# Performance work log

Measured on AMD Instinct MI355X. Metric: run time of the kernel, lower is better.

Reference implementation:

```python
import jax, jax.numpy as jnp
import numpy as np

B, N, D, H, DK, DV, R = 4, 256, 256, 8, 32, 32, 64
EPS = 1e-6


def setup_inputs() -> dict:
    key = jax.random.key(0)
    ks = jax.random.split(key, 16)
    s = D ** -0.5
    return {
        "q": jax.random.normal(ks[0], (B, N, D), jnp.float32),
        "k": jax.random.normal(ks[1], (B, N, D), jnp.float32),
        "v": jax.random.normal(ks[2], (B, N, D), jnp.float32),
        "mask": jax.random.randint(ks[3], (B, N, N), 0, 2).astype(jnp.int32),
        "link": jax.random.uniform(ks[4], (B, N, N, R), jnp.float32),
        "Wq": jax.random.normal(ks[5], (D, H * DK), jnp.float32) * s,
        "Wk": jax.random.normal(ks[6], (D, H * DK), jnp.float32) * s,
        "Wr": jax.random.normal(ks[7], (D, H * DK), jnp.float32) * s,
        "Wv": jax.random.normal(ks[8], (D, H * DV), jnp.float32) * s,
        "Wvv": jax.random.normal(ks[9], (D, H * DV), jnp.float32) * s,
        "relationE": jax.random.normal(ks[10], (R, D), jnp.float32) * s,
        "Wo": jax.random.normal(ks[11], (H * DV, D), jnp.float32) * s,
        "gamma": jnp.ones((D,), jnp.float32),
        "beta": jnp.zeros((D,), jnp.float32),
    }


def reference(q, k, v, mask, link, Wq, Wk, Wr, Wv, Wvv, relationE, Wo, gamma, beta):
    # rela_num != 0 branch of Ruleformer MultiHeadAttention (dropout = identity, eval mode).
    residual = q
    b, n, d = q.shape
    # per-head projections of X (== q == residual in this branch): [b,h,n,dk]
    Xq = (q @ Wq).reshape(b, n, H, DK).transpose(0, 2, 1, 3)
    Xk = (q @ Wk).reshape(b, n, H, DK).transpose(0, 2, 1, 3)
    Xv = (q @ Wv).reshape(b, n, H, DV).transpose(0, 2, 1, 3)

    # calcE: relation-biased scores. Rk[b,i,j,h,d] = (link @ relationE @ Wr)
    Rk = jnp.einsum('bijr,re->bije', link, relationE @ Wr).reshape(b, n, n, H, DK)
    # attn[b,h,i,j] = Xq[b,h,i] . (Xk[b,h,j] + Rk[b,i,j,h])
    attn = jnp.einsum('bhid,bhjd->bhij', Xq, Xk)
    attn = attn + jnp.einsum('bijhd,bhid->bhij', Rk, Xq)
    attn = attn / (DK ** 0.5)
    attn = jnp.where(mask[:, None, :, :] == 0, -1e9, attn)
    alpha = jax.nn.softmax(attn, axis=-1)  # [b,h,n,n]

    # calcZ: Z[b,h,i] = sum_j alpha[b,h,i,j] * (Xv[b,h,j] + Rv[b,i,j,h])
    Rv = jnp.einsum('bijr,re->bije', link, relationE @ Wvv).reshape(b, n, n, H, DV)
    Z = jnp.einsum('bhij,bhjd->bhid', alpha, Xv)
    Z = Z + jnp.einsum('bhij,bijhd->bhid', alpha, Rv)

    out = Z.transpose(0, 2, 1, 3).reshape(b, n, H * DV) @ Wo
    out = out + residual
    mu = out.mean(-1, keepdims=True)
    var = ((out - mu) ** 2).mean(-1, keepdims=True)
    out = (out - mu) * jax.lax.rsqrt(var + EPS) * gamma + beta
    return out, alpha
```

## Files before the change

### kernel.cpp

```cpp
#include <hip/hip_runtime.h>
#include <math.h>

constexpr int B_ = 4, N_ = 256, D_ = 256, H_ = 8, DK_ = 32, DV_ = 32, R_ = 64;
constexpr float SCALE_ = 0.17677669529663687f;
constexpr float EPS_ = 1e-6f;

__global__ __launch_bounds__(256) void projekev_kernel(
        const float* __restrict__ q, const float* __restrict__ Wq,
        const float* __restrict__ Wk, const float* __restrict__ Wv,
        const float* __restrict__ relE, const float* __restrict__ Wr,
        const float* __restrict__ Wvv, float* __restrict__ Xq,
        float* __restrict__ Xk, float* __restrict__ Xv,
        float* __restrict__ Ek, float* __restrict__ Ev) {
    int blk = blockIdx.x;
    int t = threadIdx.x;
    __shared__ __align__(16) float ash[32 * 65];
    __shared__ __align__(16) float bsh[32 * 64];
    const float *src, *W;
    int rowbase, cbase, ct;
    float* dstE = nullptr;
    if (blk < 192) {
        ct = blk >> 4;
        int rt = blk & 15;
        src = q; rowbase = rt * 64;
        if (ct < 4)      { W = Wq; cbase = ct * 64; }
        else if (ct < 8) { W = Wk; cbase = (ct - 4) * 64; }
        else             { W = Wv; cbase = (ct - 8) * 64; }
    } else {
        int e = blk - 192;
        src = relE; rowbase = 0; ct = -1;
        W = (e < 4) ? Wr : Wvv;
        dstE = (e < 4) ? Ek : Ev;
        cbase = (e & 3) * 64;
    }
    int ti = t >> 4, tj = t & 15;
    float acc[4][4] = {{0.f}};
    for (int kc = 0; kc < 8; ++kc) {
        __syncthreads();
#pragma unroll
        for (int kk = 0; kk < 2; ++kk) {
            int m = t + kk * 256;
            int i = m >> 3, kq = m & 7;
            float4 v = *(const float4*)(src + (size_t)(rowbase + i) * 256 + kc * 32 + kq * 4);
            ash[(kq * 4 + 0) * 65 + i] = v.x;
            ash[(kq * 4 + 1) * 65 + i] = v.y;
            ash[(kq * 4 + 2) * 65 + i] = v.z;
            ash[(kq * 4 + 3) * 65 + i] = v.w;
        }
#pragma unroll
        for (int kk = 0; kk < 2; ++kk) {
            int m = t + kk * 256;
            int k = m >> 4, j4 = m & 15;
            float4 v = *(const float4*)(W + (size_t)(kc * 32 + k) * 256 + cbase + j4 * 4);
            *(float4*)(bsh + k * 64 + j4 * 4) = v;
        }
        __syncthreads();
#pragma unroll 8
        for (int k = 0; k < 32; ++k) {
            float4 av = *(const float4*)(ash + k * 65 + ti * 4);
            float4 bv = *(const float4*)(bsh + k * 64 + tj * 4);
            acc[0][0] += av.x * bv.x; acc[0][1] += av.x * bv.y;
            acc[0][2] += av.x * bv.z; acc[0][3] += av.x * bv.w;
            acc[1][0] += av.y * bv.x; acc[1][1] += av.y * bv.y;
            acc[1][2] += av.y * bv.z; acc[1][3] += av.y * bv.w;
            acc[2][0] += av.z * bv.x; acc[2][1] += av.z * bv.y;
            acc[2][2] += av.z * bv.z; acc[2][3] += av.z * bv.w;
            acc[3][0] += av.w * bv.x; acc[3][1] += av.w * bv.y;
            acc[3][2] += av.w * bv.z; acc[3][3] += av.w * bv.w;
        }
    }
    if (dstE) {
#pragma unroll
        for (int a = 0; a < 4; ++a) {
            int row = ti * 4 + a;
            *(float4*)(dstE + (size_t)row * 256 + cbase + tj * 4) =
                make_float4(acc[a][0], acc[a][1], acc[a][2], acc[a][3]);
        }
    } else {
        float* dst = (ct < 4) ? Xq : (ct < 8) ? Xk : Xv;
        int gcol = (ct & 3) * 64 + tj * 4;
        int h = gcol >> 5, dk = gcol & 31;
#pragma unroll
        for (int a = 0; a < 4; ++a) {
            int row = rowbase + ti * 4 + a;
            int bb = row >> 8, n = row & 255;
            *(float4*)(dst + ((size_t)(bb * 8 + h) * 256 + n) * 32 + dk) =
                make_float4(acc[a][0], acc[a][1], acc[a][2], acc[a][3]);
        }
    }
}

__global__ __launch_bounds__(256, 4) void biassmzout_kernel(
        const float* __restrict__ link, const float* __restrict__ Ek,
        const float* __restrict__ Ev, const float* __restrict__ Xq,
        const float* __restrict__ Xk, const float* __restrict__ Xv,
        const int* __restrict__ mask, const float* __restrict__ Wo,
        const float* __restrict__ q, const float* __restrict__ gamma,
        const float* __restrict__ beta, float* __restrict__ alpha,
        float* __restrict__ out) {
    int bi = ((blockIdx.x & 7) << 7) | (blockIdx.x >> 3);
    int b = bi >> 8, i = bi & 255;
    int t = threadIdx.x;
    int lane = t & 63, g = t >> 6;

    __shared__ __align__(16) float xqsh[256];
    __shared__ __align__(16) float Tsh[8 * 68];
    __shared__ __align__(16) float ashm[8 * 260];
    __shared__ __align__(16) float part[2048];
    __shared__ float redsh[64];

    float resid = q[(size_t)bi * 256 + t];
    int mv = mask[((size_t)(b * 256 + i)) * 256 + t];
    xqsh[t] = Xq[((size_t)(b * 8 + (t >> 5)) * 256 + i) * 32 + (t & 31)];
    __syncthreads();

#pragma unroll
    for (int hr = t; hr < 512; hr += 256) {
        int h = hr >> 6, r = hr & 63;
        const float4* e4 = (const float4*)(Ek + r * 256 + h * 32);
        const float4* x4 = (const float4*)(xqsh + h * 32);
        float acc = 0.f;
#pragma unroll
        for (int k = 0; k < 8; ++k) {
            float4 e = e4[k], x = x4[k];
            acc += e.x * x.x + e.y * x.y + e.z * x.z + e.w * x.w;
        }
        Tsh[h * 68 + r] = acc;
    }

    float s[8];
#pragma unroll 2
    for (int h = 0; h < 8; ++h) {
        const float4* k4 = (const float4*)(Xk + (((size_t)(b * 8 + h)) * 256 + t) * 32);
        const float4* x4 = (const float4*)(xqsh + h * 32);
        float acc = 0.f;
#pragma unroll
        for (int k = 0; k < 8; ++k) {
            float4 kv = k4[k], xv = x4[k];
            acc += kv.x * xv.x + kv.y * xv.y + kv.z * xv.z + kv.w * xv.w;
        }
        s[h] = acc;
    }
    __syncthreads();

    {
        const float4* l4 = (const float4*)(link + ((size_t)(bi * 256 + t)) * 64);
        const float4* T4 = (const float4*)Tsh;
#pragma unroll 8
        for (int k = 0; k < 16; ++k) {
            float4 lv = l4[k];
#pragma unroll
            for (int h = 0; h < 8; ++h) {
                float4 tv = T4[h * 17 + k];
                s[h] += lv.x * tv.x + lv.y * tv.y + lv.z * tv.z + lv.w * tv.w;
            }
        }
    }
#pragma unroll
    for (int h = 0; h < 8; ++h) {
        s[h] *= SCALE_;
        if (mv == 0) s[h] = -1e9f;
    }

#pragma unroll
    for (int h = 0; h < 8; ++h) {
        float v = s[h];
        for (int off = 32; off > 0; off >>= 1) v = fmaxf(v, __shfl_xor(v, off));
        if (lane == 0) redsh[h * 4 + g] = v;
    }
    __syncthreads();
    float mx[8];
#pragma unroll
    for (int h = 0; h < 8; ++h)
        mx[h] = fmaxf(fmaxf(redsh[h * 4 + 0], redsh[h * 4 + 1]),
                      fmaxf(redsh[h * 4 + 2], redsh[h * 4 + 3]));
#pragma unroll
    for (int h = 0; h < 8; ++h) {
        float e = __expf(s[h] - mx[h]);
        s[h] = e;
        float v = e;
        for (int off = 32; off > 0; off >>= 1) v += __shfl_xor(v, off);
        if (lane == 0) redsh[32 + h * 4 + g] = v;
    }
    __syncthreads();
#pragma unroll
    for (int h = 0; h < 8; ++h) {
        float esum = redsh[32 + h * 4 + 0] + redsh[32 + h * 4 + 1] +
                     redsh[32 + h * 4 + 2] + redsh[32 + h * 4 + 3];
        float a = s[h] * (1.f / esum);
        ashm[h * 260 + t] = a;
        alpha[((size_t)(b * 8 + h) * 256 + i) * 256 + t] = a;
    }
    __syncthreads();

    {
        float pacc[8] = {0.f, 0.f, 0.f, 0.f, 0.f, 0.f, 0.f, 0.f};
        const float* lp2 = link + ((size_t)(bi * 256 + g * 64)) * 64 + lane;
#pragma unroll 4
        for (int j4 = 0; j4 < 16; ++j4) {
            float l0 = lp2[(j4 * 4 + 0) * 64];
            float l1 = lp2[(j4 * 4 + 1) * 64];
            float l2 = lp2[(j4 * 4 + 2) * 64];
            float l3 = lp2[(j4 * 4 + 3) * 64];
#pragma unroll
            for (int h = 0; h < 8; ++h) {
                float4 a = *(const float4*)(ashm + h * 260 + g * 64 + j4 * 4);
                pacc[h] += a.x * l0 + a.y * l1 + a.z * l2 + a.w * l3;
            }
        }
#pragma unroll
        for (int h = 0; h < 8; ++h) part[g * 512 + h * 64 + lane] = pacc[h];
    }
    __syncthreads();
    for (int hr = t; hr < 512; hr += 256)
        Tsh[(hr >> 6) * 68 + (hr & 63)] =
            part[hr] + part[512 + hr] + part[1024 + hr] + part[1536 + hr];
    __syncthreads();

    {
        int h = lane >> 3, dv4 = lane & 7;
        const float4* xv4 = (const float4*)Xv + (((size_t)(b * 8 + h)) * 256 + g * 64) * 8 + dv4;
        const float* ap = ashm + h * 260 + g * 64;
        float4 z = make_float4(0.f, 0.f, 0.f, 0.f);
#pragma unroll 8
        for (int j = 0; j < 64; ++j) {
            float a = ap[j];
            float4 x = xv4[j * 8];
            z.x += a * x.x; z.y += a * x.y; z.z += a * x.z; z.w += a * x.w;
        }
        const float4* ev4 = (const float4*)Ev + (g * 16) * 64 + h * 8 + dv4;
        const float* sp = Tsh + h * 68 + g * 16;
#pragma unroll
        for (int r = 0; r < 16; ++r) {
            float sv = sp[r];
            float4 e = ev4[r * 64];
            z.x += sv * e.x; z.y += sv * e.y; z.z += sv * e.z; z.w += sv * e.w;
        }
        ((float4*)part)[g * 64 + lane] = z;
    }
    __syncthreads();
    {
        float zv = part[t] + part[256 + t] + part[512 + t] + part[768 + t];
        ashm[t] = zv;
    }
    __syncthreads();

    float a = resid;
    {
        const float4* z4 = (const float4*)ashm;
        const float* wp = Wo + t;
#pragma unroll 4
        for (int d4 = 0; d4 < 64; ++d4) {
            float4 zz = z4[d4];
            a += zz.x * wp[(d4 * 4 + 0) * 256] + zz.y * wp[(d4 * 4 + 1) * 256] +
                 zz.z * wp[(d4 * 4 + 2) * 256] + zz.w * wp[(d4 * 4 + 3) * 256];
        }
    }
    {
        float v = a, v2 = a * a;
        for (int off = 32; off > 0; off >>= 1) {
            v += __shfl_xor(v, off);
            v2 += __shfl_xor(v2, off);
        }
        if (lane == 0) { redsh[g] = v; redsh[8 + g] = v2; }
    }
    __syncthreads();
    {
        float sum = redsh[0] + redsh[1] + redsh[2] + redsh[3];
        float sum2 = redsh[8] + redsh[9] + redsh[10] + redsh[11];
        float mu = sum * (1.f / 256.f);
        float var = sum2 * (1.f / 256.f) - mu * mu;
        out[(size_t)bi * 256 + t] = (a - mu) * rsqrtf(var + EPS_) * gamma[t] + beta[t];
    }
}

extern "C" void kernel_launch(void* const* d_in, const int* in_sizes, int n_in,
                              void* d_out, int out_size, void* d_ws, size_t ws_size,
                              hipStream_t stream) {
    const float* q     = (const float*)d_in[0];
    const int*   mask  = (const int*)d_in[3];
    const float* link  = (const float*)d_in[4];
    const float* Wq    = (const float*)d_in[5];
    const float* Wk    = (const float*)d_in[6];
    const float* Wr    = (const float*)d_in[7];
    const float* Wv    = (const float*)d_in[8];
    const float* Wvv   = (const float*)d_in[9];
    const float* relE  = (const float*)d_in[10];
    const float* Wo    = (const float*)d_in[11];
    const float* gamma = (const float*)d_in[12];
    const float* beta  = (const float*)d_in[13];

    float* out   = (float*)d_out;
    float* alpha = out + B_ * N_ * D_;

    float* ws = (float*)d_ws;
    float* Ek = ws;
    float* Ev = Ek + 16384;
    float* Xq = Ev + 16384;
    float* Xk = Xq + 262144;
    float* Xv = Xk + 262144;

    projekev_kernel<<<200, 256, 0, stream>>>(q, Wq, Wk, Wv, relE, Wr, Wvv,
                                             Xq, Xk, Xv, Ek, Ev);
    biassmzout_kernel<<<1024, 256, 0, stream>>>(link, Ek, Ev, Xq, Xk, Xv, mask,
                                                Wo, q, gamma, beta, alpha, out);
}
```

Before: 201.8 us.

## Double threads per row block in fused attention kernel, splitting heads and reductions

The fused bias/softmax/Z/output kernel now launches 512 threads per block instead of 256. Each half of the block handles four heads in the score and softmax phase, the link·alpha and Z partials are split across 8 waves, and the Wo projection is split into two halves that are then summed. The aim is more parallelism and latency hiding per row. The cost is larger shared memory, more partial-sum reduction work, and a launch bound of 8 that may force register limits. Link rows are now read by both halves of the block, so that traffic is duplicated.

```diff
diff --git a/kernel.cpp b/kernel.cpp
--- a/kernel.cpp
+++ b/kernel.cpp
@@ -90,7 +90,7 @@
     }
 }
 
-__global__ __launch_bounds__(256, 4) void biassmzout_kernel(
+__global__ __launch_bounds__(512, 8) void biassmzout_kernel(
         const float* __restrict__ link, const float* __restrict__ Ek,
         const float* __restrict__ Ev, const float* __restrict__ Xq,
         const float* __restrict__ Xk, const float* __restrict__ Xv,
@@ -101,37 +101,39 @@
     int bi = ((blockIdx.x & 7) << 7) | (blockIdx.x >> 3);
     int b = bi >> 8, i = bi & 255;
     int t = threadIdx.x;
-    int lane = t & 63, g = t >> 6;
+    int tj = t & 255;
+    int th = t >> 8;
+    int wave = t >> 6, lane = t & 63;
 
     __shared__ __align__(16) float xqsh[256];
     __shared__ __align__(16) float Tsh[8 * 68];
     __shared__ __align__(16) float ashm[8 * 260];
-    __shared__ __align__(16) float part[2048];
+    __shared__ __align__(16) float part[4096];
     __shared__ float redsh[64];
 
-    float resid = q[(size_t)bi * 256 + t];
-    int mv = mask[((size_t)(b * 256 + i)) * 256 + t];
-    xqsh[t] = Xq[((size_t)(b * 8 + (t >> 5)) * 256 + i) * 32 + (t & 31)];
-    __syncthreads();
-
-#pragma unroll
-    for (int hr = t; hr < 512; hr += 256) {
-        int h = hr >> 6, r = hr & 63;
+    float resid = q[(size_t)bi * 256 + tj];
+    int mv = mask[((size_t)(b * 256 + i)) * 256 + tj];
+    if (t < 256) xqsh[t] = Xq[((size_t)(b * 8 + (t >> 5)) * 256 + i) * 32 + (t & 31)];
+    __syncthreads();
+
+    {
+        int h = t >> 6, r = t & 63;
         const float4* e4 = (const float4*)(Ek + r * 256 + h * 32);
         const float4* x4 = (const float4*)(xqsh + h * 32);
         float acc = 0.f;
 #pragma unroll
         for (int k = 0; k < 8; ++k) {
             float4 e = e4[k], x = x4[k];
-            acc += e.x * x.x + e.y * x.y + e.z * x.z + e.w * x.w;
+            acc += e.x * x.x + e.y * x.y + e.z 	* x.z + e.w * x.w;
         }
         Tsh[h * 68 + r] = acc;
     }
 
-    float s[8];
-#pragma unroll 2
-    for (int h = 0; h < 8; ++h) {
-        const float4* k4 = (const float4*)(Xk + (((size_t)(b * 8 + h)) * 256 + t) * 32);
+    float s[4];
+#pragma unroll
+    for (int hh = 0; hh < 4; ++hh) {
+        int h = th * 4 + hh;
+        const float4* k4 = (const float4*)(Xk + (((size_t)(b * 8 + h)) * 256 + tj) * 32);
         const float4* x4 = (const float4*)(xqsh + h * 32);
         float acc = 0.f;
 #pragma unroll
@@ -139,133 +141,143 @@
             float4 kv = k4[k], xv = x4[k];
             acc += kv.x * xv.x + kv.y * xv.y + kv.z * xv.z + kv.w * xv.w;
         }
-        s[h] = acc;
-    }
-    __syncthreads();
-
-    {
-        const float4* l4 = (const float4*)(link + ((size_t)(bi * 256 + t)) * 64);
+        s[hh] = acc;
+    }
+    __syncthreads();
+
+    {
+        const float4* l4 = (const float4*)(link + (((size_t)bi * 256) + tj) * 64);
         const float4* T4 = (const float4*)Tsh;
 #pragma unroll 8
         for (int k = 0; k < 16; ++k) {
             float4 lv = l4[k];
 #pragma unroll
-            for (int h = 0; h < 8; ++h) {
-                float4 tv = T4[h * 17 + k];
-                s[h] += lv.x * tv.x + lv.y * tv.y + lv.z * tv.z + lv.w * tv.w;
+            for (int hh = 0; hh < 4; ++hh) {
+                float4 tv = T4[(th * 4 + hh) * 17 + k];
+                s[hh] += lv.x * tv.x + lv.y * tv.y + lv.z * tv.z + lv.w * tv.w;
             }
         }
     }
 #pragma unroll
-    for (int h = 0; h < 8; ++h) {
-        s[h] *= SCALE_;
-        if (mv == 0) s[h] = -1e9f;
-    }
-
-#pragma unroll
-    for (int h = 0; h < 8; ++h) {
-        float v = s[h];
+    for (int hh = 0; hh < 4; ++hh) {
+        s[hh] *= SCALE_;
+        if (mv == 0) s[hh] = -1e9f;
+    }
+
+#pragma unroll
+    for (int hh = 0; hh < 4; ++hh) {
+        float v = s[hh];
         for (int off = 32; off > 0; off >>= 1) v = fmaxf(v, __shfl_xor(v, off));
-        if (lane == 0) redsh[h * 4 + g] = v;
-    }
-    __syncthreads();
-    float mx[8];
-#pragma unroll
-    for (int h = 0; h < 8; ++h)
-        mx[h] = fmaxf(fmaxf(redsh[h * 4 + 0], redsh[h * 4 + 1]),
-                      fmaxf(redsh[h * 4 + 2], redsh[h * 4 + 3]));
-#pragma unroll
-    for (int h = 0; h < 8; ++h) {
-        float e = __expf(s[h] - mx[h]);
-        s[h] = e;
+        if (lane == 0) redsh[(th * 4 + hh) * 4 + (wave & 3)] = v;
+    }
+    __syncthreads();
+    float mx[4];
+#pragma unroll
+    for (int hh = 0; hh < 4; ++hh) {
+        const float* rp = redsh + (th * 4 + hh) * 4;
+        mx[hh] = fmaxf(fmaxf(rp[0], rp[1]), fmaxf(rp[2], rp[3]));
+    }
+#pragma unroll
+    for (int hh = 0; hh < 4; ++hh) {
+        float e = __expf(s[hh] - mx[hh]);
+        s[hh] = e;
         float v = e;
         for (int off = 32; off > 0; off >>= 1) v += __shfl_xor(v, off);
-        if (lane == 0) redsh[32 + h * 4 + g] = v;
-    }
-    __syncthreads();
-#pragma unroll
-    for (int h = 0; h < 8; ++h) {
-        float esum = redsh[32 + h * 4 + 0] + redsh[32 + h * 4 + 1] +
-                     redsh[32 + h * 4 + 2] + redsh[32 + h * 4 + 3];
-        float a = s[h] * (1.f / esum);
-        ashm[h * 260 + t] = a;
-        alpha[((size_t)(b * 8 + h) * 256 + i) * 256 + t] = a;
+        if (lane == 0) redsh[32 + (th * 4 + hh) * 4 + (wave & 3)] = v;
+    }
+    __syncthreads();
+#pragma unroll
+    for (int hh = 0; hh < 4; ++hh) {
+        int h = th * 4 + hh;
+        const float* rp = redsh + 32 + h * 4;
+        float esum = rp[0] + rp[1] + rp[2] + rp[3];
+        float a = s[hh] * (1.f / esum);
+        ashm[h * 260 + tj] = a;
+        alpha[((size_t)(b * 8 + h) * 256 + i) * 256 + tj] = a;
     }
     __syncthreads();
 
     {
         float pacc[8] = {0.f, 0.f, 0.f, 0.f, 0.f, 0.f, 0.f, 0.f};
-        const float* lp2 = link + ((size_t)(bi * 256 + g * 64)) * 64 + lane;
+        const float* lp2 = link + (((size_t)bi * 256) + wave * 32) * 64 + lane;
 #pragma unroll 4
-        for (int j4 = 0; j4 < 16; ++j4) {
+        for (int j4 = 0; j4 < 8; ++j4) {
             float l0 = lp2[(j4 * 4 + 0) * 64];
             float l1 = lp2[(j4 * 4 + 1) * 64];
             float l2 = lp2[(j4 * 4 + 2) * 64];
             float l3 = lp2[(j4 * 4 + 3) * 64];
 #pragma unroll
             for (int h = 0; h < 8; ++h) {
-                float4 a = *(const float4*)(ashm + h * 260 + g * 64 + j4 * 4);
+                float4 a = *(const float4*)(ashm + h * 260 + wave * 32 + j4 * 4);
                 pacc[h] += a.x * l0 + a.y * l1 + a.z * l2 + a.w * l3;
             }
         }
 #pragma unroll
-        for (int h = 0; h < 8; ++h) part[g * 512 + h * 64 + lane] = pacc[h];
-    }
-    __syncthreads();
-    for (int hr = t; hr < 512; hr += 256)
-        Tsh[(hr >> 6) * 68 + (hr & 63)] =
-            part[hr] + part[512 + hr] + part[1024 + hr] + part[1536 + hr];
+        for (int h = 0; h < 8; ++h) part[wave * 512 + h * 64 + lane] = pacc[h];
+    }
+    __syncthreads();
+    {
+        float v = 0.f;
+#pragma unroll
+        for (int w = 0; w < 8; ++w) v += part[w * 512 + t];
+        Tsh[(t >> 6) * 68 + (t & 63)] = v;
+    }
     __syncthreads();
 
     {
         int h = lane >> 3, dv4 = lane & 7;
-        const float4* xv4 = (const float4*)Xv + (((size_t)(b * 8 + h)) * 256 + g * 64) * 8 + dv4;
-        const float* ap = ashm + h * 260 + g * 64;
+        const float4* xv4 = (const float4*)Xv + (((size_t)(b * 8 + h)) * 256 + wave * 32) * 8 + dv4;
+        const float* ap = ashm + h * 260 + wave * 32;
         float4 z = make_float4(0.f, 0.f, 0.f, 0.f);
 #pragma unroll 8
-        for (int j = 0; j < 64; ++j) {
+        for (int j = 0; j < 32; ++j) {
             float a = ap[j];
             float4 x = xv4[j * 8];
             z.x += a * x.x; z.y += a * x.y; z.z += a * x.z; z.w += a * x.w;
         }
-        const float4* ev4 = (const float4*)Ev + (g * 16) * 64 + h * 8 + dv4;
-        const float* sp = Tsh + h * 68 + g * 16;
-#pragma unroll
-        for (int r = 0; r < 16; ++r) {
+        const float4* ev4 = (const float4*)Ev + (wave * 8) * 64 + h * 8 + dv4;
+        const float* sp = Tsh + h * 68 + wave * 8;
+#pragma unroll
+        for (int r = 0; r < 8; ++r) {
             float sv = sp[r];
             float4 e = ev4[r * 64];
             z.x += sv * e.x; z.y += sv * e.y; z.z += sv * e.z; z.w += sv * e.w;
         }
-        ((float4*)part)[g * 64 + lane] = z;
-    }
-    __syncthreads();
-    {
-        float zv = part[t] + part[256 + t] + part[512 + t] + part[768 + t];
-        ashm[t] = zv;
-    }
-    __syncthreads();
-
-    float a = resid;
-    {
-        const float4* z4 = (const float4*)ashm;
-        const float* wp = Wo + t;
+        ((float4*)part)[wave * 64 + lane] = z;
+    }
+    __syncthreads();
+    if (t < 256) {
+        float zv = 0.f;
+#pragma unroll
+        for (int w = 0; w < 8; ++w) zv += part[w * 256 + t];
+        xqsh[t] = zv;
+    }
+    __syncthreads();
+
+    {
+        float ap_ = 0.f;
+        const float4* z4 = (const float4*)xqsh;
+        const float* wp = Wo + tj;
 #pragma unroll 4
-        for (int d4 = 0; d4 < 64; ++d4) {
+        for (int d4 = th * 32; d4 < th * 32 + 32; ++d4) {
             float4 zz = z4[d4];
-            a += zz.x * wp[(d4 * 4 + 0) * 256] + zz.y * wp[(d4 * 4 + 1) * 256] +
-                 zz.z * wp[(d4 * 4 + 2) * 256] + zz.w * wp[(d4 * 4 + 3) * 256];
-        }
-    }
+            ap_ += zz.x * wp[(d4 * 4 + 0) * 256] + zz.y * wp[(d4 * 4 + 1) * 256] +
+                   zz.z * wp[(d4 * 4 + 2) * 256] + zz.w * wp[(d4 * 4 + 3) * 256];
+        }
+        part[th * 256 + tj] = ap_;
+    }
+    __syncthreads();
+    float a = part[tj] + part[256 + tj] + resid;
     {
         float v = a, v2 = a * a;
         for (int off = 32; off > 0; off >>= 1) {
             v += __shfl_xor(v, off);
             v2 += __shfl_xor(v2, off);
         }
-        if (lane == 0) { redsh[g] = v; redsh[8 + g] = v2; }
-    }
-    __syncthreads();
-    {
+        if (th == 0 && lane == 0) { redsh[wave] = v; redsh[8 + wave] = v2; }
+    }
+    __syncthreads();
+    if (t < 256) {
         float sum = redsh[0] + redsh[1] + redsh[2] + redsh[3];
         float sum2 = redsh[8] + redsh[9] + redsh[10] + redsh[11];
         float mu = sum * (1.f / 256.f);
@@ -302,6 +314,6 @@
 
     projekev_kernel<<<200, 256, 0, stream>>>(q, Wq, Wk, Wv, relE, Wr, Wvv,
                                              Xq, Xk, Xv, Ek, Ev);
-    biassmzout_kernel<<<1024, 256, 0, stream>>>(link, Ek, Ev, Xq, Xk, Xv, mask,
+    biassmzout_kernel<<<1024, 512, 0, stream>>>(link, Ek, Ev, Xq, Xk, Xv, mask,
                                                 Wo, q, gamma, beta, alpha, out);
 }
```

Result: slower. 280.7 us (+39.1%).
